# Kernel tuning notes

Hardware: AMD Instinct MI355X
Metric: run time of the kernel (lower is better)

## Reference

```python
import jax, jax.numpy as jnp
import numpy as np

LN_EPS = 1e-5


def _make_valid_boxes(key, shape):
    # boxes in [x_min, y_min, x_max, y_max] with min < max
    k1, k2 = jax.random.split(key)
    mins = jax.random.uniform(k1, shape, dtype=jnp.float32)            # [.., 2]
    sizes = jax.random.uniform(k2, shape, dtype=jnp.float32) * 0.2 + 1e-3
    return jnp.concatenate([mins, mins + sizes], axis=-1)


def setup_inputs() -> dict:
    key = jax.random.key(0)
    k_t, k_b, k_w = jax.random.split(key, 3)
    N, H = 100000, 768
    target = _make_valid_boxes(k_t, (2,))          # [4]
    ocr_boxes = _make_valid_boxes(k_b, (N, 2))     # [N, 4]
    W = jax.random.normal(k_w, (11, H), dtype=jnp.float32) * (1.0 / np.sqrt(11))
    b = jnp.zeros((H,), dtype=jnp.float32)
    ln_gamma = jnp.ones((H,), dtype=jnp.float32)
    ln_beta = jnp.zeros((H,), dtype=jnp.float32)
    return {"target": target, "ocr_boxes": ocr_boxes, "W": W, "b": b,
            "ln_gamma": ln_gamma, "ln_beta": ln_beta}


def _geo_features(target, boxes):
    # target: [4], boxes: [N, 4]  (x_min, y_min, x_max, y_max)
    tx0, ty0, tx1, ty1 = target[0], target[1], target[2], target[3]
    x0, y0, x1, y1 = boxes[:, 0], boxes[:, 1], boxes[:, 2], boxes[:, 3]
    N = boxes.shape[0]
    ones = jnp.ones((N,), boxes.dtype)

    # HeightWidthRelation: [w1, h1, w2, h2, |w1-w2|, |h1-h2|]
    w1, h1 = tx1 - tx0, ty1 - ty0
    w2, h2 = x1 - x0, y1 - y0
    hw = jnp.stack([w1 * ones, h1 * ones, w2, h2,
                    jnp.abs(w1 - w2), jnp.abs(h1 - h2)], axis=-1)   # [N, 6]

    # Centers
    c1x, c1y = (tx0 + tx1) * 0.5, (ty0 + ty1) * 0.5
    c2x, c2y = (x0 + x1) * 0.5, (y0 + y1) * 0.5
    dx, dy = c2x - c1x, c2y - c1y

    # DistanceRelation: L2 center distance
    dist = jnp.sqrt(dx * dx + dy * dy)                               # [N]

    # IoURelation
    overlap = (tx0 < x1) & (tx1 > x0) & (ty0 < y1) & (ty1 > y0)
    xi0, yi0 = jnp.maximum(tx0, x0), jnp.maximum(ty0, y0)
    xi1, yi1 = jnp.minimum(tx1, x1), jnp.minimum(ty1, y1)
    inter = jnp.where(overlap, (xi1 - xi0) * (yi1 - yi0), 0.0)       # [N]
    a1 = w1 * h1
    a2 = w2 * h2
    union = a1 + a2 - inter
    iou = jnp.stack([inter / union, inter / a1, inter / a2], axis=-1)  # [N, 3]

    # AngleRelation: atan2(|dy|, |dx|) degree bucket (degree in [0, 90])
    degree = jnp.arctan2(jnp.abs(dy), jnp.abs(dx)) * (180.0 / jnp.pi)
    bucket = jnp.where((degree > 22.5) & (degree <= 67.5), 1.0,
             jnp.where((degree > 67.5) & (degree <= 112.5), 2.0,
             jnp.where((degree > 112.5) & (degree <= 157.5), 3.0,
             jnp.where((degree > 157.5) & (degree <= 202.5), 4.0,
             jnp.where((degree > 202.5) & (degree <= 247.5), 5.0,
             jnp.where((degree > 247.5) & (degree <= 292.5), 6.0,
             jnp.where((degree > 292.5) & (degree <= 337.5), 7.0, 8.0)))))))

    return jnp.concatenate([hw, dist[:, None], iou, bucket[:, None]], axis=-1)  # [N, 11]


def reference(target, ocr_boxes, W, b, ln_gamma, ln_beta):
    feats = _geo_features(target, ocr_boxes)            # [N, 11]
    x = feats @ W + b                                   # [N, H]
    mean = jnp.mean(x, axis=-1, keepdims=True)
    var = jnp.mean(jnp.square(x - mean), axis=-1, keepdims=True)
    x = (x - mean) * jax.lax.rsqrt(var + LN_EPS) * ln_gamma + ln_beta
    return jax.nn.relu(x)
```

## Files before the change

kernel.cpp:

```cpp
#include <hip/hip_runtime.h>
#include <math.h>

#define H 768
#define LN_EPS 1e-5f

__global__ __launch_bounds__(256) void geo_ln_kernel(
    const float* __restrict__ target,
    const float* __restrict__ boxes,
    const float* __restrict__ W,
    const float* __restrict__ bias,
    const float* __restrict__ gamma,
    const float* __restrict__ beta,
    float* __restrict__ out,
    int N)
{
    const int lane = threadIdx.x & 63;
    const int wid  = (blockIdx.x << 2) | (threadIdx.x >> 6);
    const int nw   = gridDim.x << 2;

    const float tx0 = target[0], ty0 = target[1], tx1 = target[2], ty1 = target[3];
    const float w1 = tx1 - tx0, h1 = ty1 - ty0;
    const float c1x = (tx0 + tx1) * 0.5f, c1y = (ty0 + ty1) * 0.5f;
    const float a1 = w1 * h1;

    const float4* __restrict__ W4  = reinterpret_cast<const float4*>(W);
    const float4* __restrict__ b4  = reinterpret_cast<const float4*>(bias);
    const float4* __restrict__ g4  = reinterpret_cast<const float4*>(gamma);
    const float4* __restrict__ be4 = reinterpret_cast<const float4*>(beta);
    const float4* __restrict__ boxes4 = reinterpret_cast<const float4*>(boxes);
    float4* __restrict__ out4 = reinterpret_cast<float4*>(out);

    float4 base[3], Wr[3][9], gm[3], bt[3];
    #pragma unroll
    for (int r = 0; r < 3; ++r) {
        const int c4 = lane + 64 * r;
        float4 acc = b4[c4];
        const float4 w0 = W4[0 * (H / 4) + c4];
        const float4 w1r = W4[1 * (H / 4) + c4];
        acc.x = fmaf(w1, w0.x, acc.x); acc.y = fmaf(w1, w0.y, acc.y);
        acc.z = fmaf(w1, w0.z, acc.z); acc.w = fmaf(w1, w0.w, acc.w);
        acc.x = fmaf(h1, w1r.x, acc.x); acc.y = fmaf(h1, w1r.y, acc.y);
        acc.z = fmaf(h1, w1r.z, acc.z); acc.w = fmaf(h1, w1r.w, acc.w);
        base[r] = acc;
        #pragma unroll
        for (int k = 0; k < 9; ++k)
            Wr[r][k] = W4[(k + 2) * (H / 4) + c4];
        gm[r] = g4[c4];
        bt[r] = be4[c4];
    }

    for (int box = wid; box < N; box += nw) {
        const float4 bx = boxes4[box];
        const float x0 = bx.x, y0 = bx.y, x1 = bx.z, y1 = bx.w;

        float v[9];
        const float w2 = x1 - x0, h2 = y1 - y0;
        v[0] = w2; v[1] = h2;
        v[2] = fabsf(w1 - w2); v[3] = fabsf(h1 - h2);
        const float c2x = (x0 + x1) * 0.5f, c2y = (y0 + y1) * 0.5f;
        const float dx = c2x - c1x, dy = c2y - c1y;
        v[4] = sqrtf(dx * dx + dy * dy);
        const bool overlap = (tx0 < x1) && (tx1 > x0) && (ty0 < y1) && (ty1 > y0);
        const float xi0 = fmaxf(tx0, x0), yi0 = fmaxf(ty0, y0);
        const float xi1 = fminf(tx1, x1), yi1 = fminf(ty1, y1);
        const float inter = overlap ? (xi1 - xi0) * (yi1 - yi0) : 0.0f;
        const float a2 = w2 * h2;
        const float uni = a1 + a2 - inter;
        v[5] = inter / uni; v[6] = inter / a1; v[7] = inter / a2;
        const float degree = atan2f(fabsf(dy), fabsf(dx)) * 57.29577951308232f;
        v[8] = (degree > 22.5f) ? ((degree > 67.5f) ? 2.0f : 1.0f) : 8.0f;

        float4 xv[3];
        float s = 0.0f, sq = 0.0f;
        #pragma unroll
        for (int r = 0; r < 3; ++r) {
            float4 acc = base[r];
            #pragma unroll
            for (int k = 0; k < 9; ++k) {
                const float4 w = Wr[r][k];
                acc.x = fmaf(v[k], w.x, acc.x);
                acc.y = fmaf(v[k], w.y, acc.y);
                acc.z = fmaf(v[k], w.z, acc.z);
                acc.w = fmaf(v[k], w.w, acc.w);
            }
            xv[r] = acc;
            s  += acc.x + acc.y + acc.z + acc.w;
            sq += acc.x * acc.x + acc.y * acc.y + acc.z * acc.z + acc.w * acc.w;
        }

        #pragma unroll
        for (int off = 32; off >= 1; off >>= 1) {
            s  += __shfl_xor(s,  off, 64);
            sq += __shfl_xor(sq, off, 64);
        }
        const float mean = s * (1.0f / H);
        const float var  = sq * (1.0f / H) - mean * mean;
        const float rstd = rsqrtf(var + LN_EPS);

        float4* __restrict__ orow = out4 + (size_t)box * (H / 4);
        #pragma unroll
        for (int r = 0; r < 3; ++r) {
            const float4 vx = xv[r];
            const float4 g = gm[r], be = bt[r];
            float4 o;
            o.x = fmaxf(0.0f, (vx.x - mean) * rstd * g.x + be.x);
            o.y = fmaxf(0.0f, (vx.y - mean) * rstd * g.y + be.y);
            o.z = fmaxf(0.0f, (vx.z - mean) * rstd * g.z + be.z);
            o.w = fmaxf(0.0f, (vx.w - mean) * rstd * g.w + be.w);
            orow[lane + 64 * r] = o;
        }
    }
}

extern "C" void kernel_launch(void* const* d_in, const int* in_sizes, int n_in,
                              void* d_out, int out_size, void* d_ws, size_t ws_size,
                              hipStream_t stream) {
    const float* target = (const float*)d_in[0];
    const float* boxes  = (const float*)d_in[1];
    const float* W      = (const float*)d_in[2];
    const float* bias   = (const float*)d_in[3];
    const float* gamma  = (const float*)d_in[4];
    const float* beta   = (const float*)d_in[5];
    float* out = (float*)d_out;

    const int N = in_sizes[1] / 4;
    const int grid = 512;

    geo_ln_kernel<<<grid, 256, 0, stream>>>(target, boxes, W, bias, gamma, beta, out, N);
}
```

Before: 371.9 us.

## Use fast math intrinsics, tangent-based angle bucket, nontemporal stores, and 2x loop unroll

Replaces sqrt, division and rsqrt with AMDGPU hardware approximation intrinsics and precomputes 1/a1. The atan2-based angle bucket becomes comparisons of |dy| against |dx| scaled by tan(22.5°) and tan(67.5°). Output rows are written with nontemporal stores to avoid polluting cache, the box loop is unrolled by two, and launch bounds request two blocks per CU. The kernel is dominated by the output write, so the arithmetic changes may matter little. The approximate intrinsics can slightly change numerics.

Result: faster. 351.1 us (-5.6%).

```diff
diff --git a/kernel.cpp b/kernel.cpp
--- a/kernel.cpp
+++ b/kernel.cpp
@@ -4,7 +4,9 @@
 #define H 768
 #define LN_EPS 1e-5f
 
-__global__ __launch_bounds__(256) void geo_ln_kernel(
+typedef float nfloat4 __attribute__((ext_vector_type(4)));
+
+__global__ __launch_bounds__(256, 2) void geo_ln_kernel(
     const float* __restrict__ target,
     const float* __restrict__ boxes,
     const float* __restrict__ W,
@@ -22,13 +24,16 @@
     const float w1 = tx1 - tx0, h1 = ty1 - ty0;
     const float c1x = (tx0 + tx1) * 0.5f, c1y = (ty0 + ty1) * 0.5f;
     const float a1 = w1 * h1;
+    const float ra1 = 1.0f / a1;
+    const float tanA = 0.41421356237309503f;
+    const float tanB = 2.41421356237309503f;
 
     const float4* __restrict__ W4  = reinterpret_cast<const float4*>(W);
     const float4* __restrict__ b4  = reinterpret_cast<const float4*>(bias);
     const float4* __restrict__ g4  = reinterpret_cast<const float4*>(gamma);
     const float4* __restrict__ be4 = reinterpret_cast<const float4*>(beta);
     const float4* __restrict__ boxes4 = reinterpret_cast<const float4*>(boxes);
-    float4* __restrict__ out4 = reinterpret_cast<float4*>(out);
+    nfloat4* __restrict__ outv = reinterpret_cast<nfloat4*>(out);
 
     float4 base[3], Wr[3][9], gm[3], bt[3];
     #pragma unroll
@@ -49,7 +54,7 @@
         bt[r] = be4[c4];
     }
 
-    for (int box = wid; box < N; box += nw) {
+    auto process = [&](int box) {
         const float4 bx = boxes4[box];
         const float x0 = bx.x, y0 = bx.y, x1 = bx.z, y1 = bx.w;
 
@@ -59,16 +64,18 @@
         v[2] = fabsf(w1 - w2); v[3] = fabsf(h1 - h2);
         const float c2x = (x0 + x1) * 0.5f, c2y = (y0 + y1) * 0.5f;
         const float dx = c2x - c1x, dy = c2y - c1y;
-        v[4] = sqrtf(dx * dx + dy * dy);
+        v[4] = __builtin_amdgcn_sqrtf(dx * dx + dy * dy);
         const bool overlap = (tx0 < x1) && (tx1 > x0) && (ty0 < y1) && (ty1 > y0);
         const float xi0 = fmaxf(tx0, x0), yi0 = fmaxf(ty0, y0);
         const float xi1 = fminf(tx1, x1), yi1 = fminf(ty1, y1);
         const float inter = overlap ? (xi1 - xi0) * (yi1 - yi0) : 0.0f;
         const float a2 = w2 * h2;
         const float uni = a1 + a2 - inter;
-        v[5] = inter / uni; v[6] = inter / a1; v[7] = inter / a2;
-        const float degree = atan2f(fabsf(dy), fabsf(dx)) * 57.29577951308232f;
-        v[8] = (degree > 22.5f) ? ((degree > 67.5f) ? 2.0f : 1.0f) : 8.0f;
+        v[5] = inter * __builtin_amdgcn_rcpf(uni);
+        v[6] = inter * ra1;
+        v[7] = inter * __builtin_amdgcn_rcpf(a2);
+        const float adx = fabsf(dx), ady = fabsf(dy);
+        v[8] = (ady > adx * tanA) ? ((ady > adx * tanB) ? 2.0f : 1.0f) : 8.0f;
 
         float4 xv[3];
         float s = 0.0f, sq = 0.0f;
@@ -95,21 +102,28 @@
         }
         const float mean = s * (1.0f / H);
         const float var  = sq * (1.0f / H) - mean * mean;
-        const float rstd = rsqrtf(var + LN_EPS);
+        const float rstd = __builtin_amdgcn_rsqf(var + LN_EPS);
 
-        float4* __restrict__ orow = out4 + (size_t)box * (H / 4);
+        nfloat4* __restrict__ orow = outv + (size_t)box * (H / 4);
         #pragma unroll
         for (int r = 0; r < 3; ++r) {
             const float4 vx = xv[r];
             const float4 g = gm[r], be = bt[r];
-            float4 o;
+            nfloat4 o;
             o.x = fmaxf(0.0f, (vx.x - mean) * rstd * g.x + be.x);
             o.y = fmaxf(0.0f, (vx.y - mean) * rstd * g.y + be.y);
             o.z = fmaxf(0.0f, (vx.z - mean) * rstd * g.z + be.z);
             o.w = fmaxf(0.0f, (vx.w - mean) * rstd * g.w + be.w);
-            orow[lane + 64 * r] = o;
+            __builtin_nontemporal_store(o, &orow[lane + 64 * r]);
         }
+    };
+
+    int box = wid;
+    for (; box + nw < N; box += 2 * nw) {
+        process(box);
+        process(box + nw);
     }
+    if (box < N) process(box);
 }
 
 extern "C" void kernel_launch(void* const* d_in, const int* in_sizes, int n_in,
```
